# Kernel tuning notes

Hardware: AMD Instinct MI355X
Metric: run time of the kernel (lower is better)

Reference implementation:

```python
import jax, jax.numpy as jnp
import numpy as np

LN_EPS = 1e-5

def layernorm(x, g, b):
    mu = jnp.mean(x, axis=-1, keepdims=True)
    var = jnp.mean(jnp.square(x - mu), axis=-1, keepdims=True)
    return (x - mu) * jax.lax.rsqrt(var + LN_EPS) * g + b

def setup_inputs() -> dict:
    B, T, C, H = 4, 1024, 1024, 16
    hd = C // H
    key = jax.random.key(0)
    ks = jax.random.split(key, 16)
    s = 0.02
    inp = {
        "x":  jax.random.normal(ks[0], (B, T, C), jnp.float32),
        # per-head QKV projections, stacked over heads: [H, C, hd] / [H, hd]
        "Wq": jax.random.normal(ks[1], (H, C, hd), jnp.float32) * s,
        "bq": jax.random.normal(ks[2], (H, hd), jnp.float32) * s,
        "Wk": jax.random.normal(ks[3], (H, C, hd), jnp.float32) * s,
        "bk": jax.random.normal(ks[4], (H, hd), jnp.float32) * s,
        "Wv": jax.random.normal(ks[5], (H, C, hd), jnp.float32) * s,
        "bv": jax.random.normal(ks[6], (H, hd), jnp.float32) * s,
        # LayerNorm params: ln1, ln2 (decoder), lnf (inside FeedForward)
        "g1": 1.0 + jax.random.normal(ks[7], (C,), jnp.float32) * s,
        "b1": jax.random.normal(ks[8], (C,), jnp.float32) * s,
        "g2": 1.0 + jax.random.normal(ks[9], (C,), jnp.float32) * s,
        "b2": jax.random.normal(ks[10], (C,), jnp.float32) * s,
        "gf": 1.0 + jax.random.normal(ks[11], (C,), jnp.float32) * s,
        "bf": jax.random.normal(ks[12], (C,), jnp.float32) * s,
        # FFN
        "W1": jax.random.normal(ks[13], (C, 4 * C), jnp.float32) * s,
        "b1f": jnp.zeros((4 * C,), jnp.float32),
        "W2": jax.random.normal(ks[14], (4 * C, C), jnp.float32) * s,
        "b2f": jnp.zeros((C,), jnp.float32),
    }
    return inp

def reference(x, Wq, bq, Wk, bk, Wv, bv, g1, b1, g2, b2, gf, bf, W1, b1f, W2, b2f):
    B, T, C = x.shape
    h = layernorm(x, g1, b1)                      # ln1
    # multi-head causal attention (per-head projections stacked on H)
    q = jnp.einsum("btc,hcd->bhtd", h, Wq) + bq[None, :, None, :]
    k = jnp.einsum("btc,hcd->bhtd", h, Wk) + bk[None, :, None, :]
    v = jnp.einsum("btc,hcd->bhtd", h, Wv) + bv[None, :, None, :]
    # NOTE: original scales by C**-0.5 (n_embd), not head_size**-0.5
    att = jnp.einsum("bhtd,bhsd->bhts", q, k) / jnp.sqrt(jnp.float32(C))
    causal = jnp.tril(jnp.ones((T, T), bool))
    att = jnp.where(causal, att, -jnp.inf)
    att = jax.nn.softmax(att, axis=-1)
    o = jnp.einsum("bhts,bhsd->bhtd", att, v)     # [B,H,T,hd]
    o = jnp.transpose(o, (0, 2, 1, 3)).reshape(B, T, C)  # concat heads
    x2 = h + o
    x3 = layernorm(x2, g2, b2)                    # ln2
    # FeedForward: hf = ln(x3); out = net(hf) + hf  (residual uses post-LN!)
    hf = layernorm(x3, gf, bf)
    ff = jax.nn.relu(hf @ W1 + b1f) @ W2 + b2f + hf
    return x3 + ff                                # dropout is identity in eval
```

## Files before the change

### kernel.cpp

```cpp
#include <hip/hip_runtime.h>
#include <hip/hip_bf16.h>


typedef __attribute__((ext_vector_type(8))) short short8;
typedef __attribute__((ext_vector_type(4))) short short4v;
typedef __attribute__((ext_vector_type(4))) float f32x4;

#define DEVI static __device__ __forceinline__

#define BAR() __builtin_amdgcn_s_barrier()
#define SB0() __builtin_amdgcn_sched_barrier(0)

template <int N>
DEVI void vmwN() {
  asm volatile("s_waitcnt vmcnt(%0)" ::"n"(N) : "memory");
  __builtin_amdgcn_sched_barrier(0);
}
template <int N>
DEVI void lgkmN() {
  asm volatile("s_waitcnt lgkmcnt(%0)" ::"n"(N) : "memory");
  __builtin_amdgcn_sched_barrier(0);
}

DEVI void gload_lds16(const void* g, void* l) {
  __builtin_amdgcn_global_load_lds(
      (const __attribute__((address_space(1))) void*)g,
      (__attribute__((address_space(3))) void*)l, 16, 0, 0);
}

DEVI float bf2f(short s) {
  union { float f; unsigned u; } cv;
  cv.u = ((unsigned)(unsigned short)s) << 16;
  return cv.f;
}
DEVI short f2bf(float f) {
  union { float f; unsigned u; } cv;
  cv.f = f;
  unsigned u = cv.u;
  u += 0x7FFFu + ((u >> 16) & 1u);
  return (short)(u >> 16);
}

DEVI void block_reduce2(float& s, float& s2, float* red, int t) {
#pragma unroll
  for (int off = 1; off < 64; off <<= 1) {
    s += __shfl_xor(s, off, 64);
    s2 += __shfl_xor(s2, off, 64);
  }
  __syncthreads();
  if ((t & 63) == 0) { red[(t >> 6) * 2] = s; red[(t >> 6) * 2 + 1] = s2; }
  __syncthreads();
  s = red[0] + red[2] + red[4] + red[6];
  s2 = red[1] + red[3] + red[5] + red[7];
}

DEVI void xcd_swz(int gx, int gy, int& bx, int& by) {
  const int flat = blockIdx.y * gx + blockIdx.x;
  const int c = (gx * gy) >> 3;
  const int nf = (flat & 7) * c + (flat >> 3);
  bx = nf % gx;
  by = nf / gx;
}

__global__ __launch_bounds__(256) void transpose_all(
    const float* __restrict__ Wq, const float* __restrict__ Wk,
    const float* __restrict__ Wv, const float* __restrict__ W1,
    const float* __restrict__ W2, short* __restrict__ wqkv_t,
    short* __restrict__ w1_t, short* __restrict__ w2_t) {
  __shared__ float tile[32][33];
  const int bid = blockIdx.x;
  const int tx = threadIdx.x, ty = threadIdx.y;
  const float* in;
  short* o;
  int r0, c0, R, C;
  if (bid < 3072) {
    const int bx = bid & 1, rem = bid >> 1;
    const int by = rem & 31, z = rem >> 5;
    const int sel = z >> 4, b = z & 15;
    in = ((sel == 0) ? Wq : (sel == 1) ? Wk : Wv) + (size_t)b * 1024 * 64;
    o = wqkv_t + (size_t)sel * 1024 * 1024 + (size_t)b * 1024 * 64;
    r0 = by * 32; c0 = bx * 32; R = 1024; C = 64;
  } else if (bid < 7168) {
    const int b2 = bid - 3072;
    const int bx = b2 & 127, by = b2 >> 7;
    in = W1; o = w1_t;
    r0 = by * 32; c0 = bx * 32; R = 1024; C = 4096;
  } else {
    const int b2 = bid - 7168;
    const int bx = b2 & 31, by = b2 >> 5;
    in = W2; o = w2_t;
    r0 = by * 32; c0 = bx * 32; R = 4096; C = 1024;
  }
#pragma unroll
  for (int i = 0; i < 32; i += 8)
    tile[ty + i][tx] = in[(size_t)(r0 + ty + i) * C + c0 + tx];
  __syncthreads();
#pragma unroll
  for (int i = 0; i < 32; i += 8)
    o[(size_t)(c0 + ty + i) * R + r0 + tx] = f2bf(tile[tx][ty + i]);
}

__global__ __launch_bounds__(256) void ln1_kernel(
    const float* __restrict__ x, const float* __restrict__ g,
    const float* __restrict__ b, short* __restrict__ hb) {
  __shared__ float red[8];
  const int row = blockIdx.x, t = threadIdx.x;
  float4 v = ((const float4*)(x + (size_t)row * 1024))[t];
  float s = v.x + v.y + v.z + v.w;
  float s2 = v.x * v.x + v.y * v.y + v.z * v.z + v.w * v.w;
  block_reduce2(s, s2, red, t);
  const float mu = s * (1.0f / 1024.0f);
  const float rstd = rsqrtf(s2 * (1.0f / 1024.0f) - mu * mu + 1e-5f);
  float4 gv = ((const float4*)g)[t], bv = ((const float4*)b)[t];
  short4v p = {f2bf((v.x - mu) * rstd * gv.x + bv.x),
               f2bf((v.y - mu) * rstd * gv.y + bv.y),
               f2bf((v.z - mu) * rstd * gv.z + bv.z),
               f2bf((v.w - mu) * rstd * gv.w + bv.w)};
  ((short4v*)(hb + (size_t)row * 1024))[t] = p;
}

__global__ __launch_bounds__(256) void ln2f_kernel(
    const short* __restrict__ hbb, const short* __restrict__ ob,
    const float* __restrict__ g2, const float* __restrict__ b2,
    const float* __restrict__ gf, const float* __restrict__ bfp,
    short* __restrict__ x3, short* __restrict__ hfb) {
  __shared__ float red[8];
  const int row = blockIdx.x, t = threadIdx.x;
  short4v hv4 = ((const short4v*)(hbb + (size_t)row * 1024))[t];
  short4v ov4 = ((const short4v*)(ob + (size_t)row * 1024))[t];
  float4 v;
  v.x = bf2f(hv4.x) + bf2f(ov4.x);
  v.y = bf2f(hv4.y) + bf2f(ov4.y);
  v.z = bf2f(hv4.z) + bf2f(ov4.z);
  v.w = bf2f(hv4.w) + bf2f(ov4.w);
  float s = v.x + v.y + v.z + v.w;
  float s2 = v.x * v.x + v.y * v.y + v.z * v.z + v.w * v.w;
  block_reduce2(s, s2, red, t);
  float mu = s * (1.0f / 1024.0f);
  float rstd = rsqrtf(s2 * (1.0f / 1024.0f) - mu * mu + 1e-5f);
  float4 gv = ((const float4*)g2)[t], bv = ((const float4*)b2)[t];
  float4 xv;
  xv.x = (v.x - mu) * rstd * gv.x + bv.x;
  xv.y = (v.y - mu) * rstd * gv.y + bv.y;
  xv.z = (v.z - mu) * rstd * gv.z + bv.z;
  xv.w = (v.w - mu) * rstd * gv.w + bv.w;
  short4v xp = {f2bf(xv.x), f2bf(xv.y), f2bf(xv.z), f2bf(xv.w)};
  ((short4v*)(x3 + (size_t)row * 1024))[t] = xp;
  s = xv.x + xv.y + xv.z + xv.w;
  s2 = xv.x * xv.x + xv.y * xv.y + xv.z * xv.z + xv.w * xv.w;
  block_reduce2(s, s2, red, t);
  mu = s * (1.0f / 1024.0f);
  rstd = rsqrtf(s2 * (1.0f / 1024.0f) - mu * mu + 1e-5f);
  float4 gv2 = ((const float4*)gf)[t], bv2 = ((const float4*)bfp)[t];
  short4v pk = {f2bf((xv.x - mu) * rstd * gv2.x + bv2.x),
                f2bf((xv.y - mu) * rstd * gv2.y + bv2.y),
                f2bf((xv.z - mu) * rstd * gv2.z + bv2.z),
                f2bf((xv.w - mu) * rstd * gv2.w + bv2.w)};
  ((short4v*)(hfb + (size_t)row * 1024))[t] = pk;
}

template <int EPI>
DEVI void gemm8_body(const short* __restrict__ A, const short* __restrict__ B,
                     int K, int kbase, int m0, int n0,
                     const float* __restrict__ f0, const float* __restrict__ f1,
                     const float* __restrict__ f2, short* __restrict__ s0,
                     short* __restrict__ s1, short* __restrict__ s2) {
  extern __shared__ __align__(16) char lds[];
  constexpr int NT = 16;
  const int tid = threadIdx.x;
  const int l = tid & 63, w = tid >> 6;
  const int wrM = w >> 2, wcN = w & 3;
  const int lr = l & 15, lg = l >> 4;

  const int cswz = (((lr & 1) << 2) | lg) ^ (lr >> 1);
  const int laneoff = ((lr >> 1) << 7) + (cswz << 4);

  const int rsel = l >> 3;
  const int scz = (l & 7) ^ rsel;
  const int s_roff = w * 16 + rsel * 2 + (scz >> 2);
  const int s_kc = (scz & 3) * 8;
  const short* Asrc = A + (size_t)(m0 + s_roff) * K + kbase + s_kc;
  const short* Bsrc = B + (size_t)(n0 + s_roff) * K + kbase + s_kc;
  const size_t rstep = (size_t)128 * K;

  auto STAGE = [&](int op, int kh, int t) {
    const short* g = (op ? Bsrc : Asrc) + t * 64 + kh * 32;
    char* d = lds + ((t & 1) * 65536 + op * 32768 + kh * 16384 + w * 1024);
    gload_lds16(g, d);
    gload_lds16(g + rstep, d + 8192);
  };

  f32x4 acc[8][4] = {};

  STAGE(0, 0, 0); STAGE(1, 0, 0); STAGE(0, 1, 0); STAGE(1, 1, 0);
  vmwN<0>(); BAR(); SB0();

  for (int t = 0; t < NT; ++t) {
    const bool st = (t + 1) < NT;
    const char* pa0 = lds + (t & 1) * 65536 + wrM * 8192 + laneoff;
    const char* pb0 = lds + (t & 1) * 65536 + 32768 + wcN * 4096 + laneoff;
#pragma unroll
    for (int kh = 0; kh < 2; ++kh) {
      const char* pa = pa0 + kh * 16384;
      const char* pb = pb0 + kh * 16384;
      short8 a[8], b[4];
#pragma unroll
      for (int mt = 0; mt < 8; ++mt) a[mt] = *(const short8*)(pa + mt * 1024);
      b[0] = *(const short8*)(pb);
      b[1] = *(const short8*)(pb + 1024);
      SB0();
      b[2] = *(const short8*)(pb + 2048);
      b[3] = *(const short8*)(pb + 3072);
      if (kh == 0 && st) {
        STAGE(0, 0, t + 1); STAGE(1, 0, t + 1);
        STAGE(0, 1, t + 1); STAGE(1, 1, t + 1);
      }
      lgkmN<2>();
      __builtin_amdgcn_s_setprio(1);
#pragma unroll
      for (int mt = 0; mt < 8; ++mt) {
        acc[mt][0] = __builtin_amdgcn_mfma_f32_16x16x32_bf16(a[mt], b[0], acc[mt][0], 0, 0, 0);
        acc[mt][1] = __builtin_amdgcn_mfma_f32_16x16x32_bf16(a[mt], b[1], acc[mt][1], 0, 0, 0);
      }
      __builtin_amdgcn_s_setprio(0);
      lgkmN<0>();
      __builtin_amdgcn_s_setprio(1);
#pragma unroll
      for (int mt = 0; mt < 8; ++mt) {
        acc[mt][2] = __builtin_amdgcn_mfma_f32_16x16x32_bf16(a[mt], b[2], acc[mt][2], 0, 0, 0);
        acc[mt][3] = __builtin_amdgcn_mfma_f32_16x16x32_bf16(a[mt], b[3], acc[mt][3], 0, 0, 0);
      }
      __builtin_amdgcn_s_setprio(0);
    }
    if (st) vmwN<0>();
    BAR(); SB0();
  }

#pragma unroll
  for (int mt = 0; mt < 8; ++mt) {
#pragma unroll
    for (int nt = 0; nt < 4; ++nt) {
      const int col = n0 + wcN * 64 + nt * 16 + lr;
      const int row0 = m0 + wrM * 128 + mt * 16 + lg * 4;
      if constexpr (EPI == 0) {
        const int sel = col >> 10, nn = col & 1023;
        const int hh = nn >> 6, dd = nn & 63;
        const int bb = row0 >> 10, tt0 = row0 & 1023;
        if (sel == 2) {
          const float bias = f2[nn];
          short4v pk = {f2bf(acc[mt][nt][0] + bias), f2bf(acc[mt][nt][1] + bias),
                        f2bf(acc[mt][nt][2] + bias), f2bf(acc[mt][nt][3] + bias)};
          *(short4v*)&s2[(((size_t)(bb * 16 + hh)) * 64 + dd) * 1024 + tt0] = pk;
        } else {
          const float bias = (sel == 0) ? f0[nn] : f1[nn];
          short* dst = (sel == 0) ? s0 : s1;
#pragma unroll
          for (int r = 0; r < 4; ++r)
            dst[(((size_t)(bb * 16 + hh)) * 1024 + tt0 + r) * 64 + dd] =
                f2bf(acc[mt][nt][r] + bias);
        }
      } else if constexpr (EPI == 1) {
#pragma unroll
        for (int r = 0; r < 4; ++r) {
          float val = fmaxf(acc[mt][nt][r] + f0[col], 0.0f);
          s0[(size_t)(row0 + r) * 4096 + col] = f2bf(val);
        }
      } else {
#pragma unroll
        for (int r = 0; r < 4; ++r)
          s0[(size_t)(row0 + r) * 1024 + col] = f2bf(acc[mt][nt][r]);
      }
    }
  }
}

__global__ __launch_bounds__(512, 2) void gemm8_qkv(
    const short* __restrict__ A, const short* __restrict__ B,
    const float* __restrict__ bq, const float* __restrict__ bk,
    const float* __restrict__ bv, short* __restrict__ q,
    short* __restrict__ k, short* __restrict__ vt) {
  int bx, by;
  xcd_swz(12, 16, bx, by);
  gemm8_body<0>(A, B, 1024, 0, by * 256, bx * 256, bq, bk, bv, q, k, vt);
}

__global__ __launch_bounds__(512, 2) void gemm8_ffn1(
    const short* __restrict__ A, const short* __restrict__ B,
    const float* __restrict__ b1f, short* __restrict__ u) {
  int bx, by;
  xcd_swz(16, 16, bx, by);
  gemm8_body<1>(A, B, 1024, 0, by * 256, bx * 256, b1f, nullptr, nullptr, u,
                nullptr, nullptr);
}

__global__ __launch_bounds__(512, 2) void gemm8_ffn2sk(
    const short* __restrict__ A, const short* __restrict__ B,
    short* __restrict__ part) {
  const int z = blockIdx.z;
  int bx, by;
  xcd_swz(4, 16, bx, by);
  gemm8_body<2>(A, B, 4096, z * 1024, by * 256, bx * 256, nullptr, nullptr,
                nullptr, part + (size_t)z * 4096 * 1024, nullptr, nullptr);
}

__global__ __launch_bounds__(256) void ffn2_reduce(
    const short* __restrict__ part, const float* __restrict__ b2f,
    const short* __restrict__ hfb, const short* __restrict__ x3,
    float* __restrict__ out) {
  const size_t i8 = (size_t)blockIdx.x * 256 + threadIdx.x;
  const size_t S = (size_t)4096 * 1024 / 8;
  short8 a0 = ((const short8*)part)[i8];
  short8 a1 = ((const short8*)part)[i8 + S];
  short8 a2 = ((const short8*)part)[i8 + 2 * S];
  short8 a3 = ((const short8*)part)[i8 + 3 * S];
  short8 xv = ((const short8*)x3)[i8];
  short8 hv = ((const short8*)hfb)[i8];
  const int cb = (int)((i8 * 2) & 255);
  float4 bb0 = ((const float4*)b2f)[cb];
  float4 bb1 = ((const float4*)b2f)[cb + 1];
  float ob[8];
#pragma unroll
  for (int j = 0; j < 8; ++j) {
    const float bbv = j < 4 ? ((const float*)&bb0)[j] : ((const float*)&bb1)[j - 4];
    ob[j] = bf2f(a0[j]) + bf2f(a1[j]) + bf2f(a2[j]) + bf2f(a3[j]) + bbv +
            bf2f(hv[j]) + bf2f(xv[j]);
  }
  float4 o0 = {ob[0], ob[1], ob[2], ob[3]};
  float4 o1 = {ob[4], ob[5], ob[6], ob[7]};
  ((float4*)out)[i8 * 2] = o0;
  ((float4*)out)[i8 * 2 + 1] = o1;
}

__global__ __launch_bounds__(256, 5) void attn_kernel(
    const short* __restrict__ q, const short* __restrict__ k,
    const short* __restrict__ vt, short* __restrict__ o) {
  __shared__ __align__(16) short Ksm[64 * 64];
  __shared__ __align__(16) short Vsm[64 * 64];
  __shared__ __align__(16) short Psm[4 * 16 * 64];
  const int bh = blockIdx.x;
  const int qt = 15 - blockIdx.y;
  const int tid = threadIdx.x, lane = tid & 63, w = tid >> 6;
  const int lr = lane & 15, lg = lane >> 4;

  const short* qb = q + (size_t)bh * 1024 * 64;
  const short* kb = k + (size_t)bh * 1024 * 64;
  const short* vb = vt + (size_t)bh * 64 * 1024;

  const int qrow = qt * 64 + w * 16 + lr;
  short8 qf0 = *(const short8*)&qb[(size_t)qrow * 64 + lg * 8];
  short8 qf1 = *(const short8*)&qb[(size_t)qrow * 64 + 32 + lg * 8];

  f32x4 oacc[4] = {};
  float mrun = -1e30f, lrun = 0.0f;

  const float scale2 = 0.03125f * 1.44269504088896f;
  const int srow = tid >> 3;
  const int sc8 = tid & 7;
  char* pw = (char*)(Psm + w * 1024);
  const int qloc = w * 16 + lr;
  const int rowswz = (lr & 7) << 4;

  short8 kreg[2], vreg[2];
#pragma unroll
  for (int p = 0; p < 2; ++p) {
    const int rr = srow + p * 32;
    kreg[p] = *(const short8*)&kb[(size_t)rr * 64 + sc8 * 8];
    vreg[p] = *(const short8*)&vb[(size_t)rr * 1024 + sc8 * 8];
  }

  for (int kt = 0; kt <= qt; ++kt) {
#pragma unroll
    for (int p = 0; p < 2; ++p) {
      const int rr = srow + p * 32;
      *(short8*)((char*)Ksm + rr * 128 + ((sc8 ^ (rr & 7)) << 4)) = kreg[p];
      *(short8*)((char*)Vsm + rr * 128 + ((sc8 ^ (rr & 7)) << 4)) = vreg[p];
    }
    __syncthreads();
    if (kt < qt) {
#pragma unroll
      for (int p = 0; p < 2; ++p) {
        const int rr = srow + p * 32;
        kreg[p] =
            *(const short8*)&kb[((size_t)((kt + 1) * 64 + rr)) * 64 + sc8 * 8];
        vreg[p] =
            *(const short8*)&vb[(size_t)rr * 1024 + (kt + 1) * 64 + sc8 * 8];
      }
    }

    f32x4 sfr[4];
#pragma unroll
    for (int nt = 0; nt < 4; ++nt) {
      const int krow = nt * 16 + lr;
      short8 kf0 = *(const short8*)((const char*)Ksm + krow * 128 +
                                    (((0 + lg) ^ (krow & 7)) << 4));
      short8 kf1 = *(const short8*)((const char*)Ksm + krow * 128 +
                                    (((4 + lg) ^ (krow & 7)) << 4));
      f32x4 z = {};
      z = __builtin_amdgcn_mfma_f32_16x16x32_bf16(kf0, qf0, z, 0, 0, 0);
      z = __builtin_amdgcn_mfma_f32_16x16x32_bf16(kf1, qf1, z, 0, 0, 0);
      sfr[nt] = z;
    }
    if (kt == qt) {
#pragma unroll
      for (int nt = 0; nt < 4; ++nt) {
        const int kb0 = nt * 16 + lg * 4;
#pragma unroll
        for (int r = 0; r < 4; ++r)
          sfr[nt][r] = (kb0 + r <= qloc) ? sfr[nt][r] * scale2 : -1e30f;
      }
    } else {
#pragma unroll
      for (int nt = 0; nt < 4; ++nt)
#pragma unroll
        for (int r = 0; r < 4; ++r) sfr[nt][r] *= scale2;
    }
    float pm;
    {
      float a0 = fmaxf(fmaxf(sfr[0][0], sfr[0][1]), fmaxf(sfr[0][2], sfr[0][3]));
      float a1 = fmaxf(fmaxf(sfr[1][0], sfr[1][1]), fmaxf(sfr[1][2], sfr[1][3]));
      float a2 = fmaxf(fmaxf(sfr[2][0], sfr[2][1]), fmaxf(sfr[2][2], sfr[2][3]));
      float a3 = fmaxf(fmaxf(sfr[3][0], sfr[3][1]), fmaxf(sfr[3][2], sfr[3][3]));
      pm = fmaxf(fmaxf(a0, a1), fmaxf(a2, a3));
      pm = fmaxf(pm, __shfl_xor(pm, 16, 64));
      pm = fmaxf(pm, __shfl_xor(pm, 32, 64));
    }
    if (!__all(pm - mrun <= 8.0f)) {
      const float mnew = fmaxf(mrun, pm);
      const float alpha = exp2f(mrun - mnew);
      mrun = mnew;
      lrun *= alpha;
#pragma unroll
      for (int nt = 0; nt < 4; ++nt)
#pragma unroll
        for (int r = 0; r < 4; ++r) oacc[nt][r] *= alpha;
    }
    float rs;
    {
#pragma unroll
      for (int nt = 0; nt < 4; ++nt)
#pragma unroll
        for (int r = 0; r < 4; ++r) sfr[nt][r] = exp2f(sfr[nt][r] - mrun);
      float s0 = (sfr[0][0] + sfr[0][1]) + (sfr[0][2] + sfr[0][3]);
      float s1 = (sfr[1][0] + sfr[1][1]) + (sfr[1][2] + sfr[1][3]);
      float s2 = (sfr[2][0] + sfr[2][1]) + (sfr[2][2] + sfr[2][3]);
      float s3 = (sfr[3][0] + sfr[3][1]) + (sfr[3][2] + sfr[3][3]);
      rs = (s0 + s1) + (s2 + s3);
      rs += __shfl_xor(rs, 16, 64);
      rs += __shfl_xor(rs, 32, 64);
    }
    lrun += rs;

#pragma unroll
    for (int nt = 0; nt < 4; ++nt) {
      unsigned w0, w1;
      asm("v_cvt_pk_bf16_f32 %0, %1, %2"
          : "=v"(w0) : "v"(sfr[nt][0]), "v"(sfr[nt][1]));
      asm("v_cvt_pk_bf16_f32 %0, %1, %2"
          : "=v"(w1) : "v"(sfr[nt][2]), "v"(sfr[nt][3]));
      uint2 pk2 = {w0, w1};
      *(uint2*)(pw + lr * 128 + ((nt * 32 + lg * 8) ^ rowswz)) = pk2;
    }

#pragma unroll
    for (int kc = 0; kc < 2; ++kc) {
      short8 pb8 = *(const short8*)(pw + lr * 128 + ((kc * 64 + lg * 16) ^ rowswz));
#pragma unroll
      for (int nt = 0; nt < 4; ++nt) {
        const int vrow = nt * 16 + lr;
        short8 vf = *(const short8*)((const char*)Vsm + vrow * 128 +
                                     (((kc * 4 + lg) ^ (vrow & 7)) << 4));
        oacc[nt] = __builtin_amdgcn_mfma_f32_16x16x32_bf16(vf, pb8, oacc[nt], 0, 0, 0);
      }
    }
    __syncthreads();
  }

  const float inv = 1.0f / lrun;
  short* ob = o + (size_t)(bh >> 4) * 1024 * 1024 +
              (size_t)(qt * 64 + qloc) * 1024 + (bh & 15) * 64;
#pragma unroll
  for (int nt = 0; nt < 4; ++nt) {
    short4v pk = {f2bf(oacc[nt][0] * inv), f2bf(oacc[nt][1] * inv),
                  f2bf(oacc[nt][2] * inv), f2bf(oacc[nt][3] * inv)};
    *(short4v*)&ob[nt * 16 + lg * 4] = pk;
  }
}

extern "C" void kernel_launch(void* const* d_in, const int* in_sizes, int n_in,
                              void* d_out, int out_size, void* d_ws,
                              size_t ws_size, hipStream_t stream) {
  const float* x = (const float*)d_in[0];
  const float* Wq = (const float*)d_in[1];
  const float* bq = (const float*)d_in[2];
  const float* Wk = (const float*)d_in[3];
  const float* bk = (const float*)d_in[4];
  const float* Wv = (const float*)d_in[5];
  const float* bv = (const float*)d_in[6];
  const float* g1 = (const float*)d_in[7];
  const float* b1 = (const float*)d_in[8];
  const float* g2 = (const float*)d_in[9];
  const float* b2 = (const float*)d_in[10];
  const float* gf = (const float*)d_in[11];
  const float* bfp = (const float*)d_in[12];
  const float* W1 = (const float*)d_in[13];
  const float* b1f = (const float*)d_in[14];
  const float* W2 = (const float*)d_in[15];
  const float* b2f = (const float*)d_in[16];
  float* out = (float*)d_out;

  (void)hipFuncSetAttribute((const void*)gemm8_qkv,
                            hipFuncAttributeMaxDynamicSharedMemorySize, 131072);
  (void)hipFuncSetAttribute((const void*)gemm8_ffn1,
                            hipFuncAttributeMaxDynamicSharedMemorySize, 131072);
  (void)hipFuncSetAttribute((const void*)gemm8_ffn2sk,
                            hipFuncAttributeMaxDynamicSharedMemorySize, 131072);

  const size_t MB = 1024 * 1024;
  char* p = (char*)d_ws;
  short* qbuf = (short*)(p + 0 * MB);
  short* kbuf = (short*)(p + 8 * MB);
  short* vtb = (short*)(p + 16 * MB);
  short* obuf = (short*)(p + 24 * MB);
  short* wqkv_t = (short*)(p + 32 * MB);
  short* w1_t = (short*)(p + 40 * MB);
  short* part = (short*)(p + 0 * MB);
  char* q = p + 48 * MB;
  short* w2_t = (short*)(q + 0 * MB);
  short* hbb = (short*)(q + 8 * MB);
  short* x3b = (short*)(q + 16 * MB);
  short* hfb = (short*)(q + 24 * MB);
  short* ub = (short*)(q + 32 * MB);

  transpose_all<<<11264, dim3(32, 8), 0, stream>>>(Wq, Wk, Wv, W1, W2, wqkv_t,
                                                   w1_t, w2_t);

  ln1_kernel<<<4096, 256, 0, stream>>>(x, g1, b1, hbb);

  gemm8_qkv<<<dim3(12, 16), 512, 131072, stream>>>(hbb, wqkv_t, bq, bk, bv,
                                                   qbuf, kbuf, vtb);

  attn_kernel<<<dim3(64, 16), 256, 0, stream>>>(qbuf, kbuf, vtb, obuf);

  ln2f_kernel<<<4096, 256, 0, stream>>>(hbb, obuf, g2, b2, gf, bfp, x3b, hfb);

  gemm8_ffn1<<<dim3(16, 16), 512, 131072, stream>>>(hfb, w1_t, b1f, ub);

  gemm8_ffn2sk<<<dim3(4, 16, 4), 512, 131072, stream>>>(ub, w2_t, part);

  ffn2_reduce<<<2048, 256, 0, stream>>>(part, b2f, hfb, x3b, out);
}
```

Measured before the change: 172.5 us.

## Overlap W1/W2 weight transposes with QKV GEMM in a fused launch

The W1 and W2 fp32-to-bf16 transposes move out of the standalone transpose kernel into 64 extra blocks of the QKV GEMM launch, so that work runs on CUs the GEMM's 192 tiles leave idle. The standalone transpose kernel now handles only the QKV weights. The fused kernel's launch bounds drop from two to one block per CU, and each transpose block loops over 64 tiles with barriers. The XCD swizzle helper is inlined with constants in the FFN kernels.

```diff
diff --git a/kernel.cpp b/kernel.cpp
--- a/kernel.cpp
+++ b/kernel.cpp
@@ -54,50 +54,26 @@
   s2 = red[1] + red[3] + red[5] + red[7];
 }
 
-DEVI void xcd_swz(int gx, int gy, int& bx, int& by) {
-  const int flat = blockIdx.y * gx + blockIdx.x;
-  const int c = (gx * gy) >> 3;
-  const int nf = (flat & 7) * c + (flat >> 3);
-  bx = nf % gx;
-  by = nf / gx;
-}
-
-__global__ __launch_bounds__(256) void transpose_all(
+__global__ __launch_bounds__(256) void transpose_qkvw(
     const float* __restrict__ Wq, const float* __restrict__ Wk,
-    const float* __restrict__ Wv, const float* __restrict__ W1,
-    const float* __restrict__ W2, short* __restrict__ wqkv_t,
-    short* __restrict__ w1_t, short* __restrict__ w2_t) {
+    const float* __restrict__ Wv, short* __restrict__ wqkv_t) {
   __shared__ float tile[32][33];
   const int bid = blockIdx.x;
   const int tx = threadIdx.x, ty = threadIdx.y;
-  const float* in;
-  short* o;
-  int r0, c0, R, C;
-  if (bid < 3072) {
-    const int bx = bid & 1, rem = bid >> 1;
-    const int by = rem & 31, z = rem >> 5;
-    const int sel = z >> 4, b = z & 15;
-    in = ((sel == 0) ? Wq : (sel == 1) ? Wk : Wv) + (size_t)b * 1024 * 64;
-    o = wqkv_t + (size_t)sel * 1024 * 1024 + (size_t)b * 1024 * 64;
-    r0 = by * 32; c0 = bx * 32; R = 1024; C = 64;
-  } else if (bid < 7168) {
-    const int b2 = bid - 3072;
-    const int bx = b2 & 127, by = b2 >> 7;
-    in = W1; o = w1_t;
-    r0 = by * 32; c0 = bx * 32; R = 1024; C = 4096;
-  } else {
-    const int b2 = bid - 7168;
-    const int bx = b2 & 31, by = b2 >> 5;
-    in = W2; o = w2_t;
-    r0 = by * 32; c0 = bx * 32; R = 4096; C = 1024;
-  }
+  const int bx = bid & 1, rem = bid >> 1;
+  const int by = rem & 31, z = rem >> 5;
+  const int sel = z >> 4, b = z & 15;
+  const float* in =
+      ((sel == 0) ? Wq : (sel == 1) ? Wk : Wv) + (size_t)b * 1024 * 64;
+  short* o = wqkv_t + (size_t)sel * 1024 * 1024 + (size_t)b * 1024 * 64;
+  const int r0 = by * 32, c0 = bx * 32;
 #pragma unroll
   for (int i = 0; i < 32; i += 8)
-    tile[ty + i][tx] = in[(size_t)(r0 + ty + i) * C + c0 + tx];
+    tile[ty + i][tx] = in[(size_t)(r0 + ty + i) * 64 + c0 + tx];
   __syncthreads();
 #pragma unroll
   for (int i = 0; i < 32; i += 8)
-    o[(size_t)(c0 + ty + i) * R + r0 + tx] = f2bf(tile[tx][ty + i]);
+    o[(size_t)(c0 + ty + i) * 1024 + r0 + tx] = f2bf(tile[tx][ty + i]);
 }
 
 __global__ __launch_bounds__(256) void ln1_kernel(
@@ -274,21 +250,49 @@
   }
 }
 
-__global__ __launch_bounds__(512, 2) void gemm8_qkv(
+__global__ __launch_bounds__(512, 1) void gemm8_qkv_fused(
     const short* __restrict__ A, const short* __restrict__ B,
     const float* __restrict__ bq, const float* __restrict__ bk,
     const float* __restrict__ bv, short* __restrict__ q,
-    short* __restrict__ k, short* __restrict__ vt) {
-  int bx, by;
-  xcd_swz(12, 16, bx, by);
-  gemm8_body<0>(A, B, 1024, 0, by * 256, bx * 256, bq, bk, bv, q, k, vt);
+    short* __restrict__ k, short* __restrict__ vt,
+    const float* __restrict__ W1, const float* __restrict__ W2,
+    short* __restrict__ w1_t, short* __restrict__ w2_t) {
+  const int flat = blockIdx.y * 16 + blockIdx.x;
+  if (flat < 192) {
+    const int nf = (flat & 7) * 24 + (flat >> 3);
+    const int bx = nf % 12, by = nf / 12;
+    gemm8_body<0>(A, B, 1024, 0, by * 256, bx * 256, bq, bk, bv, q, k, vt);
+    return;
+  }
+  extern __shared__ __align__(16) char lds[];
+  const int tid = threadIdx.x;
+  const int unit = tid >> 8, lt = tid & 255;
+  const int tx = lt & 31, ty = lt >> 5;
+  float* tile = (float*)lds + unit * (32 * 33);
+  const int base = (flat - 192) * 2 + unit;
+  for (int it = 0; it < 64; ++it) {
+    const int tix = base + it * 128;
+    const float* in; short* o; int R, C, bx, by;
+    if (tix < 4096) { in = W1; o = w1_t; R = 1024; C = 4096; bx = tix & 127; by = tix >> 7; }
+    else { const int t2 = tix - 4096; in = W2; o = w2_t; R = 4096; C = 1024; bx = t2 & 31; by = t2 >> 5; }
+    const int r0 = by * 32, c0 = bx * 32;
+#pragma unroll
+    for (int i = 0; i < 32; i += 8)
+      tile[(ty + i) * 33 + tx] = in[(size_t)(r0 + ty + i) * C + c0 + tx];
+    __syncthreads();
+#pragma unroll
+    for (int i = 0; i < 32; i += 8)
+      o[(size_t)(c0 + ty + i) * R + r0 + tx] = f2bf(tile[tx * 33 + ty + i]);
+    __syncthreads();
+  }
 }
 
 __global__ __launch_bounds__(512, 2) void gemm8_ffn1(
     const short* __restrict__ A, const short* __restrict__ B,
     const float* __restrict__ b1f, short* __restrict__ u) {
-  int bx, by;
-  xcd_swz(16, 16, bx, by);
+  const int flat = blockIdx.y * 16 + blockIdx.x;
+  const int nf = (flat & 7) * 32 + (flat >> 3);
+  const int bx = nf & 15, by = nf >> 4;
   gemm8_body<1>(A, B, 1024, 0, by * 256, bx * 256, b1f, nullptr, nullptr, u,
                 nullptr, nullptr);
 }
@@ -297,8 +301,9 @@
     const short* __restrict__ A, const short* __restrict__ B,
     short* __restrict__ part) {
   const int z = blockIdx.z;
-  int bx, by;
-  xcd_swz(4, 16, bx, by);
+  const int flat = blockIdx.y * 4 + blockIdx.x;
+  const int nf = (flat & 7) * 8 + (flat >> 3);
+  const int bx = nf & 3, by = nf >> 2;
   gemm8_body<2>(A, B, 4096, z * 1024, by * 256, bx * 256, nullptr, nullptr,
                 nullptr, part + (size_t)z * 4096 * 1024, nullptr, nullptr);
 }
@@ -508,7 +513,7 @@
   const float* b2f = (const float*)d_in[16];
   float* out = (float*)d_out;
 
-  (void)hipFuncSetAttribute((const void*)gemm8_qkv,
+  (void)hipFuncSetAttribute((const void*)gemm8_qkv_fused,
                             hipFuncAttributeMaxDynamicSharedMemorySize, 131072);
   (void)hipFuncSetAttribute((const void*)gemm8_ffn1,
                             hipFuncAttributeMaxDynamicSharedMemorySize, 131072);
@@ -531,13 +536,12 @@
   short* hfb = (short*)(q + 24 * MB);
   short* ub = (short*)(q + 32 * MB);
 
-  transpose_all<<<11264, dim3(32, 8), 0, stream>>>(Wq, Wk, Wv, W1, W2, wqkv_t,
-                                                   w1_t, w2_t);
+  transpose_qkvw<<<3072, dim3(32, 8), 0, stream>>>(Wq, Wk, Wv, wqkv_t);
 
   ln1_kernel<<<4096, 256, 0, stream>>>(x, g1, b1, hbb);
 
-  gemm8_qkv<<<dim3(12, 16), 512, 131072, stream>>>(hbb, wqkv_t, bq, bk, bv,
-                                                   qbuf, kbuf, vtb);
+  gemm8_qkv_fused<<<dim3(16, 16), 512, 131072, stream>>>(
+      hbb, wqkv_t, bq, bk, bv, qbuf, kbuf, vtb, W1, W2, w1_t, w2_t);
 
   attn_kernel<<<dim3(64, 16), 256, 0, stream>>>(qbuf, kbuf, vtb, obuf);
 
```

Result: no change. 174.8 us (+1.3%).

## Load GEMM A-operand fragments directly from global into registers, stage only B in LDS

Applied to the files above, without the earlier changes.

The GEMM main loop no longer stages the A tile through LDS. Each wave loads its A MFMA fragments straight from global memory into registers once per K-step, and only B stays double-buffered in LDS. This halves LDS use per block (128KB to 64KB), which could allow two blocks per CU and removes the A-side LDS reads and waits. The cost is uncoalesced 16-byte global loads, A data duplicated across the four column waves, and global latency now sitting directly in front of the MFMAs with no prefetch.

```diff
diff --git a/kernel.cpp b/kernel.cpp
--- a/kernel.cpp
+++ b/kernel.cpp
@@ -14,11 +14,6 @@
 template <int N>
 DEVI void vmwN() {
   asm volatile("s_waitcnt vmcnt(%0)" ::"n"(N) : "memory");
-  __builtin_amdgcn_sched_barrier(0);
-}
-template <int N>
-DEVI void lgkmN() {
-  asm volatile("s_waitcnt lgkmcnt(%0)" ::"n"(N) : "memory");
   __builtin_amdgcn_sched_barrier(0);
 }
 
@@ -179,56 +174,49 @@
   const int scz = (l & 7) ^ rsel;
   const int s_roff = w * 16 + rsel * 2 + (scz >> 2);
   const int s_kc = (scz & 3) * 8;
-  const short* Asrc = A + (size_t)(m0 + s_roff) * K + kbase + s_kc;
   const short* Bsrc = B + (size_t)(n0 + s_roff) * K + kbase + s_kc;
   const size_t rstep = (size_t)128 * K;
 
-  auto STAGE = [&](int op, int kh, int t) {
-    const short* g = (op ? Bsrc : Asrc) + t * 64 + kh * 32;
-    char* d = lds + ((t & 1) * 65536 + op * 32768 + kh * 16384 + w * 1024);
+  const short* Afrag = A + (size_t)(m0 + wrM * 128 + lr) * K + kbase + lg * 8;
+  const size_t amt = (size_t)16 * K;
+
+  auto STAGE_B = [&](int kh, int t) {
+    const short* g = Bsrc + t * 64 + kh * 32;
+    char* d = lds + ((t & 1) * 32768 + kh * 16384 + w * 1024);
     gload_lds16(g, d);
     gload_lds16(g + rstep, d + 8192);
   };
 
   f32x4 acc[8][4] = {};
 
-  STAGE(0, 0, 0); STAGE(1, 0, 0); STAGE(0, 1, 0); STAGE(1, 1, 0);
+  STAGE_B(0, 0); STAGE_B(1, 0);
   vmwN<0>(); BAR(); SB0();
 
   for (int t = 0; t < NT; ++t) {
     const bool st = (t + 1) < NT;
-    const char* pa0 = lds + (t & 1) * 65536 + wrM * 8192 + laneoff;
-    const char* pb0 = lds + (t & 1) * 65536 + 32768 + wcN * 4096 + laneoff;
+    const char* pb0 = lds + (t & 1) * 32768 + wcN * 4096 + laneoff;
+    short8 a0[8], a1[8];
+#pragma unroll
+    for (int mt = 0; mt < 8; ++mt)
+      a0[mt] = *(const short8*)(Afrag + mt * amt + t * 64);
+#pragma unroll
+    for (int mt = 0; mt < 8; ++mt)
+      a1[mt] = *(const short8*)(Afrag + mt * amt + t * 64 + 32);
+    if (st) { STAGE_B(0, t + 1); STAGE_B(1, t + 1); }
 #pragma unroll
     for (int kh = 0; kh < 2; ++kh) {
-      const char* pa = pa0 + kh * 16384;
       const char* pb = pb0 + kh * 16384;
-      short8 a[8], b[4];
-#pragma unroll
-      for (int mt = 0; mt < 8; ++mt) a[mt] = *(const short8*)(pa + mt * 1024);
-      b[0] = *(const short8*)(pb);
-      b[1] = *(const short8*)(pb + 1024);
-      SB0();
-      b[2] = *(const short8*)(pb + 2048);
-      b[3] = *(const short8*)(pb + 3072);
-      if (kh == 0 && st) {
-        STAGE(0, 0, t + 1); STAGE(1, 0, t + 1);
-        STAGE(0, 1, t + 1); STAGE(1, 1, t + 1);
-      }
-      lgkmN<2>();
+      short8 b[4];
+#pragma unroll
+      for (int nt = 0; nt < 4; ++nt) b[nt] = *(const short8*)(pb + nt * 1024);
       __builtin_amdgcn_s_setprio(1);
 #pragma unroll
       for (int mt = 0; mt < 8; ++mt) {
-        acc[mt][0] = __builtin_amdgcn_mfma_f32_16x16x32_bf16(a[mt], b[0], acc[mt][0], 0, 0, 0);
-        acc[mt][1] = __builtin_amdgcn_mfma_f32_16x16x32_bf16(a[mt], b[1], acc[mt][1], 0, 0, 0);
-      }
-      __builtin_amdgcn_s_setprio(0);
-      lgkmN<0>();
-      __builtin_amdgcn_s_setprio(1);
-#pragma unroll
-      for (int mt = 0; mt < 8; ++mt) {
-        acc[mt][2] = __builtin_amdgcn_mfma_f32_16x16x32_bf16(a[mt], b[2], acc[mt][2], 0, 0, 0);
-        acc[mt][3] = __builtin_amdgcn_mfma_f32_16x16x32_bf16(a[mt], b[3], acc[mt][3], 0, 0, 0);
+        const short8 am = kh ? a1[mt] : a0[mt];
+        acc[mt][0] = __builtin_amdgcn_mfma_f32_16x16x32_bf16(am, b[0], acc[mt][0], 0, 0, 0);
+        acc[mt][1] = __builtin_amdgcn_mfma_f32_16x16x32_bf16(am, b[1], acc[mt][1], 0, 0, 0);
+        acc[mt][2] = __builtin_amdgcn_mfma_f32_16x16x32_bf16(am, b[2], acc[mt][2], 0, 0, 0);
+        acc[mt][3] = __builtin_amdgcn_mfma_f32_16x16x32_bf16(am, b[3], acc[mt][3], 0, 0, 0);
       }
       __builtin_amdgcn_s_setprio(0);
     }
@@ -509,11 +497,11 @@
   float* out = (float*)d_out;
 
   (void)hipFuncSetAttribute((const void*)gemm8_qkv,
-                            hipFuncAttributeMaxDynamicSharedMemorySize, 131072);
+                            hipFuncAttributeMaxDynamicSharedMemorySize, 65536);
   (void)hipFuncSetAttribute((const void*)gemm8_ffn1,
-                            hipFuncAttributeMaxDynamicSharedMemorySize, 131072);
+                            hipFuncAttributeMaxDynamicSharedMemorySize, 65536);
   (void)hipFuncSetAttribute((const void*)gemm8_ffn2sk,
-                            hipFuncAttributeMaxDynamicSharedMemorySize, 131072);
+                            hipFuncAttributeMaxDynamicSharedMemorySize, 65536);
 
   const size_t MB = 1024 * 1024;
   char* p = (char*)d_ws;
@@ -536,16 +524,16 @@
 
   ln1_kernel<<<4096, 256, 0, stream>>>(x, g1, b1, hbb);
 
-  gemm8_qkv<<<dim3(12, 16), 512, 131072, stream>>>(hbb, wqkv_t, bq, bk, bv,
-                                                   qbuf, kbuf, vtb);
+  gemm8_qkv<<<dim3(12, 16), 512, 65536, stream>>>(hbb, wqkv_t, bq, bk, bv,
+                                                  qbuf, kbuf, vtb);
 
   attn_kernel<<<dim3(64, 16), 256, 0, stream>>>(qbuf, kbuf, vtb, obuf);
 
   ln2f_kernel<<<4096, 256, 0, stream>>>(hbb, obuf, g2, b2, gf, bfp, x3b, hfb);
 
-  gemm8_ffn1<<<dim3(16, 16), 512, 131072, stream>>>(hfb, w1_t, b1f, ub);
-
-  gemm8_ffn2sk<<<dim3(4, 16, 4), 512, 131072, stream>>>(ub, w2_t, part);
+  gemm8_ffn1<<<dim3(16, 16), 512, 65536, stream>>>(hfb, w1_t, b1f, ub);
+
+  gemm8_ffn2sk<<<dim3(4, 16, 4), 512, 65536, stream>>>(ub, w2_t, part);
 
   ffn2_reduce<<<2048, 256, 0, stream>>>(part, b2f, hfb, x3b, out);
 }
```

After: 316.0 us. 83.2% more time.
